# Performance work log

Measured on AMD Instinct MI355X. Metric: run time of the kernel, lower is better.

## Reference

```python
import jax, jax.numpy as jnp
import numpy as np

B, N, E, DJ, DE = 1024, 400, 128, 128, 128  # batch, nodes, edges, joint dim, edge dim (E must equal DJ and DE for BatchNorm1d on 3D input)
BN_EPS = 1e-5


def setup_inputs() -> dict:
    key = jax.random.key(0)
    ks = jax.random.split(key, 8)
    gout = jax.random.normal(ks[0], (B, N, DJ), dtype=jnp.float32)
    eout = jax.random.normal(ks[1], (B, E, DE), dtype=jnp.float32)
    start_shift = jax.random.uniform(ks[2], (B, E, N), dtype=jnp.float32)
    end_shift = jax.random.uniform(ks[3], (B, E, N), dtype=jnp.float32)
    # Linear params: nn.init.normal_(std=0.001), bias 0
    W1 = 0.001 * jax.random.normal(ks[4], (DJ, 2 * DJ), dtype=jnp.float32)
    b1 = jnp.zeros((DJ,), dtype=jnp.float32)
    W2 = 0.001 * jax.random.normal(ks[5], (DE, DJ), dtype=jnp.float32)
    b2 = jnp.zeros((DE,), dtype=jnp.float32)
    # BatchNorm affine params: weight=1, bias=0
    g1 = jnp.ones((DJ,), dtype=jnp.float32)
    beta1 = jnp.zeros((DJ,), dtype=jnp.float32)
    g2 = jnp.ones((DE,), dtype=jnp.float32)
    beta2 = jnp.zeros((DE,), dtype=jnp.float32)
    return {"gout": gout, "eout": eout, "start_shift": start_shift, "end_shift": end_shift,
            "W1": W1, "b1": b1, "W2": W2, "b2": b2,
            "g1": g1, "beta1": beta1, "g2": g2, "beta2": beta2}


def batchnorm1d(x, gamma, beta):
    # PyTorch BatchNorm1d on 3D input: channels at dim 1, biased variance over dims (0, 2)
    mean = jnp.mean(x, axis=(0, 2), keepdims=True)
    var = jnp.mean(jnp.square(x - mean), axis=(0, 2), keepdims=True)
    xhat = (x - mean) * jax.lax.rsqrt(var + BN_EPS)
    return xhat * gamma[None, :, None] + beta[None, :, None]


def reference(gout, eout, start_shift, end_shift, W1, b1, W2, b2, g1, beta1, g2, beta2):
    # node -> edge gather via dense shift matmuls: [B,E,N] @ [B,N,DJ] -> [B,E,DJ]
    start_nodes = jnp.matmul(start_shift, gout)
    end_nodes = jnp.matmul(end_shift, gout)
    x = jnp.concatenate([start_nodes, end_nodes], axis=2)  # [B, E, 2*DJ]
    h = jnp.einsum('bef,df->bed', x, W1) + b1  # Linear(2*DJ -> DJ)
    h = jax.nn.relu(batchnorm1d(h, g1, beta1))
    h = jnp.einsum('bed,od->beo', h, W2) + b2  # Linear(DJ -> DE)
    res = batchnorm1d(h, g2, beta2)
    return jax.nn.relu(eout + res)
```

## Files before the change

kernel.cpp:

```cpp
#include <hip/hip_runtime.h>
#include <stdint.h>

#define BB 1024
#define NN 400
#define EE 128
#define DD 128
#define NSLOT 64
#define GTS2 232
#define KH0 224
#define KH1 192

typedef float f32x4 __attribute__((ext_vector_type(4)));
typedef short bf16x8 __attribute__((ext_vector_type(8)));

__device__ __forceinline__ short f2bf(float f) {
    uint32_t u = __builtin_bit_cast(uint32_t, f);
    u += 0x7fffu + ((u >> 16) & 1u);
    return (short)(u >> 16);
}

__device__ __forceinline__ float bf2f(short s) {
    return __builtin_bit_cast(float, (uint32_t)((uint16_t)s) << 16);
}

__device__ __forceinline__ bf16x8 cvt8(const f32x4 a, const f32x4 b) {
    bf16x8 r;
    r[0] = f2bf(a[0]); r[1] = f2bf(a[1]); r[2] = f2bf(a[2]); r[3] = f2bf(a[3]);
    r[4] = f2bf(b[0]); r[5] = f2bf(b[1]); r[6] = f2bf(b[2]); r[7] = f2bf(b[3]);
    return r;
}

__global__ __launch_bounds__(256)
void k0_cvtw(const float* __restrict__ W1, const float* __restrict__ W2,
             unsigned short* __restrict__ W1b, unsigned short* __restrict__ W2b)
{
    int i = blockIdx.x * 256 + threadIdx.x;
    if (i < 32768) W1b[i] = (unsigned short)f2bf(W1[i]);
    if (i < 16384) W2b[i] = (unsigned short)f2bf(W2[i]);
}

__global__ __launch_bounds__(1024, 8)
void k1_gemm(const float* __restrict__ gout, const float* __restrict__ ss,
             const float* __restrict__ es, const unsigned short* __restrict__ W1b,
             const float* __restrict__ b1, unsigned short* __restrict__ h,
             float* __restrict__ stats1)
{
    __shared__ short lds[32768];
    short* GT = lds;
    short* Ps = lds;

    const int b   = blockIdx.x;
    const int t   = threadIdx.x;
    const int w   = t >> 6;
    const int l   = t & 63;
    const int l15 = l & 15;
    const int l4  = l >> 4;
    const int kkoff = l4 * 8;

    const int arow = (w & 7) * 16 + l15;
    const float* abase = ((w < 8) ? ss : es) + ((size_t)b * EE + arow) * NN;

    f32x4 pa0 = *(const f32x4*)(abase + kkoff);
    f32x4 pa1 = *(const f32x4*)(abase + kkoff + 4);
    f32x4 pb0 = *(const f32x4*)(abase + 32 + kkoff);
    f32x4 pb1 = *(const f32x4*)(abase + 32 + kkoff + 4);

    const float* gb = gout + (size_t)b * NN * DD + (t & 127);
    auto stage = [&](int koff, int nq) {
        const int qb = t >> 7;
        short* row = &GT[(t & 127) * GTS2];
        for (int q = qb; q < nq; q += 8) {
            int kg = koff + 4 * q;
            float v0 = (kg     < NN) ? gb[(size_t)(kg)     * DD] : 0.f;
            float v1 = (kg + 1 < NN) ? gb[(size_t)(kg + 1) * DD] : 0.f;
            float v2 = (kg + 2 < NN) ? gb[(size_t)(kg + 2) * DD] : 0.f;
            float v3 = (kg + 3 < NN) ? gb[(size_t)(kg + 3) * DD] : 0.f;
            uint32_t lo = (uint32_t)(uint16_t)f2bf(v0) | ((uint32_t)(uint16_t)f2bf(v1) << 16);
            uint32_t hi = (uint32_t)(uint16_t)f2bf(v2) | ((uint32_t)(uint16_t)f2bf(v3) << 16);
            *(uint64_t*)&row[4 * q] = ((uint64_t)hi << 32) | lo;
        }
    };

    stage(0, KH0 / 4);
    __syncthreads();

    f32x4 acc[8];
#pragma unroll
    for (int cf = 0; cf < 8; ++cf) acc[cf] = f32x4{0.f, 0.f, 0.f, 0.f};

#pragma unroll
    for (int s = 0; s < 13; ++s) {
        if (s == 7) {
            __syncthreads();
            stage(KH0, KH1 / 4);
            __syncthreads();
        }
        bf16x8 a = cvt8(pa0, pa1);
        pa0 = pb0; pa1 = pb1;
        const int sn = s + 2;
        if (sn < 12) {
            pb0 = *(const f32x4*)(abase + sn * 32 + kkoff);
            pb1 = *(const f32x4*)(abase + sn * 32 + kkoff + 4);
        } else if (sn == 12) {
            int kk = 384 + kkoff;
            pb0 = f32x4{0.f, 0.f, 0.f, 0.f};
            pb1 = f32x4{0.f, 0.f, 0.f, 0.f};
            if (kk < NN)     pb0 = *(const f32x4*)(abase + kk);
            if (kk + 4 < NN) pb1 = *(const f32x4*)(abase + kk + 4);
        }
        const int k0 = (s < 7 ? s * 32 : (s - 7) * 32) + kkoff;
#pragma unroll
        for (int cf = 0; cf < 8; ++cf) {
            bf16x8 gf = *(const bf16x8*)&GT[(cf * 16 + l15) * GTS2 + k0];
            acc[cf] = __builtin_amdgcn_mfma_f32_16x16x32_bf16(a, gf, acc[cf], 0, 0, 0);
        }
    }
    __syncthreads();

#pragma unroll
    for (int cf = 0; cf < 8; ++cf)
#pragma unroll
        for (int r = 0; r < 4; ++r) {
            int row = w * 16 + l4 * 4 + r;
            int col = cf * 16 + l15;
            Ps[row * 128 + (((col >> 3) ^ (row & 7)) << 3) + (col & 7)] = f2bf(acc[cf][r]);
        }
    __syncthreads();

    const int mt = w >> 1;
    const int jh = w & 1;
    f32x4 acc2[4];
#pragma unroll
    for (int cf = 0; cf < 4; ++cf) acc2[cf] = f32x4{0.f, 0.f, 0.f, 0.f};

#pragma unroll
    for (int kf = 0; kf < 8; ++kf) {
        int roff = (kf >= 4) ? 128 : 0;
        int kcol = (kf & 3) * 32 + l4 * 8;
        int row  = roff + mt * 16 + l15;
        int cb   = kcol >> 3;
        bf16x8 xf = *(const bf16x8*)&Ps[row * 128 + ((cb ^ (row & 7)) << 3)];
#pragma unroll
        for (int cf = 0; cf < 4; ++cf) {
            int j = jh * 64 + cf * 16 + l15;
            bf16x8 wf = *(const bf16x8*)&W1b[(size_t)j * 256 + kf * 32 + l4 * 8];
            acc2[cf] = __builtin_amdgcn_mfma_f32_16x16x32_bf16(xf, wf, acc2[cf], 0, 0, 0);
        }
    }
    __syncthreads();

    float* red = (float*)lds;
    float s_r[4] = {0.f, 0.f, 0.f, 0.f};
    float q_r[4] = {0.f, 0.f, 0.f, 0.f};
#pragma unroll
    for (int cf = 0; cf < 4; ++cf) {
        float bv = b1[jh * 64 + cf * 16 + l15];
        f32x4 v = acc2[cf] + bv;
#pragma unroll
        for (int r = 0; r < 4; ++r) {
            int e = mt * 16 + l4 * 4 + r;
            h[((size_t)b * EE + e) * DD + jh * 64 + cf * 16 + l15] = (unsigned short)f2bf(v[r]);
            s_r[r] += v[r];
            q_r[r] += v[r] * v[r];
        }
    }
#pragma unroll
    for (int r = 0; r < 4; ++r) {
        float s = s_r[r], q = q_r[r];
        s += __shfl_xor(s, 1); s += __shfl_xor(s, 2); s += __shfl_xor(s, 4); s += __shfl_xor(s, 8);
        q += __shfl_xor(q, 1); q += __shfl_xor(q, 2); q += __shfl_xor(q, 4); q += __shfl_xor(q, 8);
        if (l15 == 0) {
            int e = mt * 16 + l4 * 4 + r;
            red[(e << 1) | jh]         = s;
            red[256 + ((e << 1) | jh)] = q;
        }
    }
    __syncthreads();
    if (t < 128) {
        float s = red[2 * t] + red[2 * t + 1];
        float q = red[256 + 2 * t] + red[256 + 2 * t + 1];
        int slot = b & (NSLOT - 1);
        atomicAdd(&stats1[slot * 256 + t], s);
        atomicAdd(&stats1[slot * 256 + 128 + t], q);
    }
}

__global__ __launch_bounds__(256, 4)
void k3_gemm(unsigned short* h, const unsigned short* __restrict__ W2b,
             const float* __restrict__ b2, const float* __restrict__ g1,
             const float* __restrict__ bt1,
             const float* __restrict__ stats1, float* __restrict__ stats2)
{
    __shared__ short Xs[128 * 128];
    __shared__ float sc[128];
    __shared__ float sh[128];
    const int b   = blockIdx.x;
    const int t   = threadIdx.x;
    const int w   = t >> 6;
    const int l15 = t & 15;
    const int l4  = (t >> 4) & 3;

    if (t < 128) {
        float sm = 0.f, sq = 0.f;
#pragma unroll 8
        for (int sl = 0; sl < NSLOT; ++sl) {
            sm += stats1[sl * 256 + t];
            sq += stats1[sl * 256 + 128 + t];
        }
        const float inv_n = 1.0f / (1024.0f * 128.0f);
        float m    = sm * inv_n;
        float var  = sq * inv_n - m * m;
        float rstd = rsqrtf(var + 1e-5f);
        float s    = rstd * g1[t];
        sc[t] = s;
        sh[t] = bt1[t] - m * s;
    }
    __syncthreads();

    {
        const int c8 = t & 15;
        const int eb = t >> 4;
#pragma unroll
        for (int p = 0; p < 8; ++p) {
            int e = eb + 16 * p;
            bf16x8 v8 = *(const bf16x8*)&h[((size_t)b * EE + e) * DD + c8 * 8];
            float s = sc[e], s0 = sh[e];
            bf16x8 o;
#pragma unroll
            for (int i = 0; i < 8; ++i)
                o[i] = f2bf(fmaxf(fmaf(bf2f(v8[i]), s, s0), 0.0f));
            *(bf16x8*)&Xs[e * 128 + ((c8 ^ (e & 7)) << 3)] = o;
        }
    }
    __syncthreads();

    f32x4 acc[8][2];
#pragma unroll
    for (int i = 0; i < 8; ++i) {
        acc[i][0] = f32x4{0.f, 0.f, 0.f, 0.f};
        acc[i][1] = f32x4{0.f, 0.f, 0.f, 0.f};
    }
#pragma unroll
    for (int kf = 0; kf < 4; ++kf) {
        const int k0 = kf * 32;
        const int cb = (k0 >> 3) + l4;
        bf16x8 af[8];
#pragma unroll
        for (int rf = 0; rf < 8; ++rf) {
            int row = rf * 16 + l15;
            af[rf] = *(const bf16x8*)&Xs[row * 128 + ((cb ^ (row & 7)) * 8)];
        }
#pragma unroll
        for (int cf = 0; cf < 2; ++cf) {
            int j = w * 32 + cf * 16 + l15;
            bf16x8 bfr = *(const bf16x8*)&W2b[(size_t)j * 128 + k0 + l4 * 8];
#pragma unroll
            for (int rf = 0; rf < 8; ++rf)
                acc[rf][cf] = __builtin_amdgcn_mfma_f32_16x16x32_bf16(af[rf], bfr, acc[rf][cf], 0, 0, 0);
        }
    }

    __syncthreads();
    float* red = (float*)Xs;
    const float bj0 = b2[w * 32 + l15];
    const float bj1 = b2[w * 32 + 16 + l15];
    const int j0 = w * 32 + l15;
#pragma unroll
    for (int rf = 0; rf < 8; ++rf) {
        f32x4 v0 = acc[rf][0] + bj0;
        f32x4 v1 = acc[rf][1] + bj1;
        int elb = rf * 16 + l4 * 4;
#pragma unroll
        for (int r = 0; r < 4; ++r) {
            unsigned short* op = h + (size_t)(b * EE + elb + r) * DD;
            op[j0]      = (unsigned short)f2bf(v0[r]);
            op[j0 + 16] = (unsigned short)f2bf(v1[r]);
            float s = v0[r] + v1[r];
            float q = v0[r] * v0[r] + v1[r] * v1[r];
            s += __shfl_xor(s, 1); s += __shfl_xor(s, 2); s += __shfl_xor(s, 4); s += __shfl_xor(s, 8);
            q += __shfl_xor(q, 1); q += __shfl_xor(q, 2); q += __shfl_xor(q, 4); q += __shfl_xor(q, 8);
            if (l15 == 0) {
                red[(elb + r) * 4 + w]       = s;
                red[512 + (elb + r) * 4 + w] = q;
            }
        }
    }
    __syncthreads();
    if (t < 128) {
        float s = red[t * 4] + red[t * 4 + 1] + red[t * 4 + 2] + red[t * 4 + 3];
        float q = red[512 + t * 4] + red[512 + t * 4 + 1] + red[512 + t * 4 + 2] + red[512 + t * 4 + 3];
        int slot = b & (NSLOT - 1);
        atomicAdd(&stats2[slot * 256 + t], s);
        atomicAdd(&stats2[slot * 256 + 128 + t], q);
    }
}

__global__ __launch_bounds__(256)
void k5_final(const unsigned short* __restrict__ h2, const float* __restrict__ eout,
              const float* __restrict__ g2, const float* __restrict__ bt2,
              float* __restrict__ out, const float* __restrict__ stats2)
{
    __shared__ float sc[128];
    __shared__ float sh[128];
    const int t = threadIdx.x;
    if (t < 128) {
        float sm = 0.f, sq = 0.f;
#pragma unroll 8
        for (int sl = 0; sl < NSLOT; ++sl) {
            sm += stats2[sl * 256 + t];
            sq += stats2[sl * 256 + 128 + t];
        }
        const float inv_n = 1.0f / (1024.0f * 128.0f);
        float m    = sm * inv_n;
        float var  = sq * inv_n - m * m;
        float rstd = rsqrtf(var + 1e-5f);
        float s    = rstd * g2[t];
        sc[t] = s;
        sh[t] = bt2[t] - m * s;
    }
    __syncthreads();

    const int total8 = BB * EE * DD / 8;
    for (int i8 = blockIdx.x * blockDim.x + t; i8 < total8; i8 += gridDim.x * blockDim.x) {
        int e = (i8 >> 4) & 127;
        bf16x8 v8 = *(const bf16x8*)(h2 + (size_t)i8 * 8);
        f32x4 u0 = *(const f32x4*)(eout + (size_t)i8 * 8);
        f32x4 u1 = *(const f32x4*)(eout + (size_t)i8 * 8 + 4);
        float s = sc[e], s0 = sh[e];
        f32x4 o0, o1;
#pragma unroll
        for (int i = 0; i < 4; ++i) {
            o0[i] = fmaxf(u0[i] + fmaf(bf2f(v8[i]), s, s0), 0.0f);
            o1[i] = fmaxf(u1[i] + fmaf(bf2f(v8[i + 4]), s, s0), 0.0f);
        }
        *(f32x4*)(out + (size_t)i8 * 8)     = o0;
        *(f32x4*)(out + (size_t)i8 * 8 + 4) = o1;
    }
}

extern "C" void kernel_launch(void* const* d_in, const int* in_sizes, int n_in,
                              void* d_out, int out_size, void* d_ws, size_t ws_size,
                              hipStream_t stream)
{
    const float* gout  = (const float*)d_in[0];
    const float* eout  = (const float*)d_in[1];
    const float* ss    = (const float*)d_in[2];
    const float* es    = (const float*)d_in[3];
    const float* W1    = (const float*)d_in[4];
    const float* b1    = (const float*)d_in[5];
    const float* W2    = (const float*)d_in[6];
    const float* b2    = (const float*)d_in[7];
    const float* g1    = (const float*)d_in[8];
    const float* bt1   = (const float*)d_in[9];
    const float* g2    = (const float*)d_in[10];
    const float* bt2   = (const float*)d_in[11];

    float* stats1 = (float*)d_ws;
    float* stats2 = stats1 + NSLOT * 256;
    unsigned short* W1b = (unsigned short*)(stats2 + NSLOT * 256);
    unsigned short* W2b = W1b + 32768;
    unsigned short* h   = W2b + 16384;
    float* out    = (float*)d_out;

    hipMemsetAsync((void*)stats1, 0, 2 * NSLOT * 256 * sizeof(float), stream);
    k0_cvtw<<<dim3(128), dim3(256), 0, stream>>>(W1, W2, W1b, W2b);
    k1_gemm<<<dim3(BB), dim3(1024), 0, stream>>>(gout, ss, es, W1b, b1, h, stats1);
    k3_gemm<<<dim3(BB), dim3(256), 0, stream>>>(h, W2b, b2, g1, bt1, stats1, stats2);
    k5_final<<<dim3(2048), dim3(256), 0, stream>>>(h, eout, g2, bt2, out, stats2);
}
```

Before: 272.8 us.

## Split node-gather GEMM and W1 linear into two kernels via global scratch

The fused k1 kernel is split into two. k1a stages the whole transposed gout tile (all 400 nodes) into a larger LDS buffer in one pass, which removes the mid-loop restage and its barriers. It then writes the bf16 start/end products to global scratch, borrowing the output buffer. A new k1b kernel with 256 threads reloads those products and runs the W1 linear with a wider per-wave tile, then computes the BN1 statistics. This trades an extra 64KB-per-batch global round trip and one more launch for simpler staging and different occupancy. The larger LDS footprint of k1a (about 106KB) may limit how many blocks fit per CU.

```diff
diff --git a/kernel.cpp b/kernel.cpp
--- a/kernel.cpp
+++ b/kernel.cpp
@@ -6,9 +6,7 @@
 #define EE 128
 #define DD 128
 #define NSLOT 64
-#define GTS2 232
-#define KH0 224
-#define KH1 192
+#define GTS 424
 
 typedef float f32x4 __attribute__((ext_vector_type(4)));
 typedef short bf16x8 __attribute__((ext_vector_type(8)));
@@ -39,15 +37,13 @@
     if (i < 16384) W2b[i] = (unsigned short)f2bf(W2[i]);
 }
 
-__global__ __launch_bounds__(1024, 8)
-void k1_gemm(const float* __restrict__ gout, const float* __restrict__ ss,
-             const float* __restrict__ es, const unsigned short* __restrict__ W1b,
-             const float* __restrict__ b1, unsigned short* __restrict__ h,
-             float* __restrict__ stats1)
-{
-    __shared__ short lds[32768];
+__global__ __launch_bounds__(1024, 1)
+void k1a_gemm(const float* __restrict__ gout, const float* __restrict__ ss,
+              const float* __restrict__ es, unsigned short* __restrict__ Pg)
+{
+    __shared__ short lds[54272];
     short* GT = lds;
-    short* Ps = lds;
+    short* Pl = lds;
 
     const int b   = blockIdx.x;
     const int t   = threadIdx.x;
@@ -65,12 +61,12 @@
     f32x4 pb0 = *(const f32x4*)(abase + 32 + kkoff);
     f32x4 pb1 = *(const f32x4*)(abase + 32 + kkoff + 4);
 
-    const float* gb = gout + (size_t)b * NN * DD + (t & 127);
-    auto stage = [&](int koff, int nq) {
+    {
+        const float* gb = gout + (size_t)b * NN * DD + (t & 127);
         const int qb = t >> 7;
-        short* row = &GT[(t & 127) * GTS2];
-        for (int q = qb; q < nq; q += 8) {
-            int kg = koff + 4 * q;
+        short* row = &GT[(t & 127) * GTS];
+        for (int q = qb; q < 106; q += 8) {
+            int kg = 4 * q;
             float v0 = (kg     < NN) ? gb[(size_t)(kg)     * DD] : 0.f;
             float v1 = (kg + 1 < NN) ? gb[(size_t)(kg + 1) * DD] : 0.f;
             float v2 = (kg + 2 < NN) ? gb[(size_t)(kg + 2) * DD] : 0.f;
@@ -79,9 +75,7 @@
             uint32_t hi = (uint32_t)(uint16_t)f2bf(v2) | ((uint32_t)(uint16_t)f2bf(v3) << 16);
             *(uint64_t*)&row[4 * q] = ((uint64_t)hi << 32) | lo;
         }
-    };
-
-    stage(0, KH0 / 4);
+    }
     __syncthreads();
 
     f32x4 acc[8];
@@ -90,11 +84,6 @@
 
 #pragma unroll
     for (int s = 0; s < 13; ++s) {
-        if (s == 7) {
-            __syncthreads();
-            stage(KH0, KH1 / 4);
-            __syncthreads();
-        }
         bf16x8 a = cvt8(pa0, pa1);
         pa0 = pb0; pa1 = pb1;
         const int sn = s + 2;
@@ -108,10 +97,10 @@
             if (kk < NN)     pb0 = *(const f32x4*)(abase + kk);
             if (kk + 4 < NN) pb1 = *(const f32x4*)(abase + kk + 4);
         }
-        const int k0 = (s < 7 ? s * 32 : (s - 7) * 32) + kkoff;
+        const int k0 = s * 32 + kkoff;
 #pragma unroll
         for (int cf = 0; cf < 8; ++cf) {
-            bf16x8 gf = *(const bf16x8*)&GT[(cf * 16 + l15) * GTS2 + k0];
+            bf16x8 gf = *(const bf16x8*)&GT[(cf * 16 + l15) * GTS + k0];
             acc[cf] = __builtin_amdgcn_mfma_f32_16x16x32_bf16(a, gf, acc[cf], 0, 0, 0);
         }
     }
@@ -123,62 +112,96 @@
         for (int r = 0; r < 4; ++r) {
             int row = w * 16 + l4 * 4 + r;
             int col = cf * 16 + l15;
-            Ps[row * 128 + (((col >> 3) ^ (row & 7)) << 3) + (col & 7)] = f2bf(acc[cf][r]);
-        }
-    __syncthreads();
-
-    const int mt = w >> 1;
-    const int jh = w & 1;
-    f32x4 acc2[4];
-#pragma unroll
-    for (int cf = 0; cf < 4; ++cf) acc2[cf] = f32x4{0.f, 0.f, 0.f, 0.f};
-
+            Pl[row * 128 + (((col >> 3) ^ (row & 7)) << 3) + (col & 7)] = f2bf(acc[cf][r]);
+        }
+    __syncthreads();
+
+    unsigned short* pg = Pg + (size_t)b * 32768;
+#pragma unroll
+    for (int i = 0; i < 4; ++i) {
+        int idx = i * 1024 + t;
+        bf16x8 v = *(const bf16x8*)&lds[idx * 8];
+        *(bf16x8*)&pg[idx * 8] = v;
+    }
+}
+
+__global__ __launch_bounds__(256, 2)
+void k1b_stage2(const unsigned short* __restrict__ Pg,
+                const unsigned short* __restrict__ W1b,
+                const float* __restrict__ b1, unsigned short* __restrict__ h,
+                float* __restrict__ stats1)
+{
+    __shared__ short Ps[32768];
+    const int b   = blockIdx.x;
+    const int t   = threadIdx.x;
+    const int w   = t >> 6;
+    const int l15 = t & 15;
+    const int l4  = (t >> 4) & 3;
+
+    const unsigned short* pg = Pg + (size_t)b * 32768;
+#pragma unroll
+    for (int i = 0; i < 16; ++i) {
+        int idx = i * 256 + t;
+        bf16x8 v = *(const bf16x8*)&pg[idx * 8];
+        *(bf16x8*)&Ps[idx * 8] = v;
+    }
+    __syncthreads();
+
+    f32x4 acc[8][2];
+#pragma unroll
+    for (int i = 0; i < 8; ++i) {
+        acc[i][0] = f32x4{0.f, 0.f, 0.f, 0.f};
+        acc[i][1] = f32x4{0.f, 0.f, 0.f, 0.f};
+    }
 #pragma unroll
     for (int kf = 0; kf < 8; ++kf) {
-        int roff = (kf >= 4) ? 128 : 0;
-        int kcol = (kf & 3) * 32 + l4 * 8;
-        int row  = roff + mt * 16 + l15;
-        int cb   = kcol >> 3;
-        bf16x8 xf = *(const bf16x8*)&Ps[row * 128 + ((cb ^ (row & 7)) << 3)];
-#pragma unroll
-        for (int cf = 0; cf < 4; ++cf) {
-            int j = jh * 64 + cf * 16 + l15;
+        const int roff = (kf >= 4) ? 128 : 0;
+        const int cb   = (kf & 3) * 4 + l4;
+        bf16x8 af[8];
+#pragma unroll
+        for (int rf = 0; rf < 8; ++rf) {
+            int row = roff + rf * 16 + l15;
+            af[rf] = *(const bf16x8*)&Ps[row * 128 + ((cb ^ (row & 7)) << 3)];
+        }
+#pragma unroll
+        for (int cf = 0; cf < 2; ++cf) {
+            int j = w * 32 + cf * 16 + l15;
             bf16x8 wf = *(const bf16x8*)&W1b[(size_t)j * 256 + kf * 32 + l4 * 8];
-            acc2[cf] = __builtin_amdgcn_mfma_f32_16x16x32_bf16(xf, wf, acc2[cf], 0, 0, 0);
-        }
-    }
-    __syncthreads();
-
-    float* red = (float*)lds;
-    float s_r[4] = {0.f, 0.f, 0.f, 0.f};
-    float q_r[4] = {0.f, 0.f, 0.f, 0.f};
-#pragma unroll
-    for (int cf = 0; cf < 4; ++cf) {
-        float bv = b1[jh * 64 + cf * 16 + l15];
-        f32x4 v = acc2[cf] + bv;
+#pragma unroll
+            for (int rf = 0; rf < 8; ++rf)
+                acc[rf][cf] = __builtin_amdgcn_mfma_f32_16x16x32_bf16(af[rf], wf, acc[rf][cf], 0, 0, 0);
+        }
+    }
+
+    __syncthreads();
+    float* red = (float*)Ps;
+    const float bj0 = b1[w * 32 + l15];
+    const float bj1 = b1[w * 32 + 16 + l15];
+    const int j0 = w * 32 + l15;
+#pragma unroll
+    for (int rf = 0; rf < 8; ++rf) {
+        f32x4 v0 = acc[rf][0] + bj0;
+        f32x4 v1 = acc[rf][1] + bj1;
+        int elb = rf * 16 + l4 * 4;
 #pragma unroll
         for (int r = 0; r < 4; ++r) {
-            int e = mt * 16 + l4 * 4 + r;
-            h[((size_t)b * EE + e) * DD + jh * 64 + cf * 16 + l15] = (unsigned short)f2bf(v[r]);
-            s_r[r] += v[r];
-            q_r[r] += v[r] * v[r];
-        }
-    }
-#pragma unroll
-    for (int r = 0; r < 4; ++r) {
-        float s = s_r[r], q = q_r[r];
-        s += __shfl_xor(s, 1); s += __shfl_xor(s, 2); s += __shfl_xor(s, 4); s += __shfl_xor(s, 8);
-        q += __shfl_xor(q, 1); q += __shfl_xor(q, 2); q += __shfl_xor(q, 4); q += __shfl_xor(q, 8);
-        if (l15 == 0) {
-            int e = mt * 16 + l4 * 4 + r;
-            red[(e << 1) | jh]         = s;
-            red[256 + ((e << 1) | jh)] = q;
+            unsigned short* hp = h + (size_t)(b * EE + elb + r) * DD;
+            hp[j0]      = (unsigned short)f2bf(v0[r]);
+            hp[j0 + 16] = (unsigned short)f2bf(v1[r]);
+            float s = v0[r] + v1[r];
+            float q = v0[r] * v0[r] + v1[r] * v1[r];
+            s += __shfl_xor(s, 1); s += __shfl_xor(s, 2); s += __shfl_xor(s, 4); s += __shfl_xor(s, 8);
+            q += __shfl_xor(q, 1); q += __shfl_xor(q, 2); q += __shfl_xor(q, 4); q += __shfl_xor(q, 8);
+            if (l15 == 0) {
+                red[(elb + r) * 4 + w]       = s;
+                red[512 + (elb + r) * 4 + w] = q;
+            }
         }
     }
     __syncthreads();
     if (t < 128) {
-        float s = red[2 * t] + red[2 * t + 1];
-        float q = red[256 + 2 * t] + red[256 + 2 * t + 1];
+        float s = red[t * 4] + red[t * 4 + 1] + red[t * 4 + 2] + red[t * 4 + 3];
+        float q = red[512 + t * 4] + red[512 + t * 4 + 1] + red[512 + t * 4 + 2] + red[512 + t * 4 + 3];
         int slot = b & (NSLOT - 1);
         atomicAdd(&stats1[slot * 256 + t], s);
         atomicAdd(&stats1[slot * 256 + 128 + t], q);
@@ -360,11 +383,13 @@
     unsigned short* W1b = (unsigned short*)(stats2 + NSLOT * 256);
     unsigned short* W2b = W1b + 32768;
     unsigned short* h   = W2b + 16384;
+    unsigned short* Pg  = (unsigned short*)d_out;
     float* out    = (float*)d_out;
 
     hipMemsetAsync((void*)stats1, 0, 2 * NSLOT * 256 * sizeof(float), stream);
     k0_cvtw<<<dim3(128), dim3(256), 0, stream>>>(W1, W2, W1b, W2b);
-    k1_gemm<<<dim3(BB), dim3(1024), 0, stream>>>(gout, ss, es, W1b, b1, h, stats1);
+    k1a_gemm<<<dim3(BB), dim3(1024), 0, stream>>>(gout, ss, es, Pg);
+    k1b_stage2<<<dim3(BB), dim3(256), 0, stream>>>(Pg, W1b, b1, h, stats1);
     k3_gemm<<<dim3(BB), dim3(256), 0, stream>>>(h, W2b, b2, g1, bt1, stats1, stats2);
     k5_final<<<dim3(2048), dim3(256), 0, stream>>>(h, eout, g2, bt2, out, stats2);
 }
```

New measurement: 262.8 us. 1.04x faster.

## Stream shift-matrix tiles into LDS via async global_load_lds triple buffering

Applied to the files above, without the earlier changes.

Replaces the register-prefetched loads of the start/end shift matrices with direct global-to-LDS asynchronous loads into a three-stage ring buffer, using vmcnt waits to overlap loads with the MFMA loop. The A tiles are XOR-swizzled in LDS to avoid bank conflicts, and LDS usage grows to about 154KB per block. This frees registers and hides memory latency, but it also changes the launch bound occupancy hint and adds reliance on waitcnt-based synchronization without barriers between waves. That is safe only because each wave reads only the data it loaded itself.

```diff
diff --git a/kernel.cpp b/kernel.cpp
--- a/kernel.cpp
+++ b/kernel.cpp
@@ -7,8 +7,6 @@
 #define DD 128
 #define NSLOT 64
 #define GTS2 232
-#define KH0 224
-#define KH1 192
 
 typedef float f32x4 __attribute__((ext_vector_type(4)));
 typedef short bf16x8 __attribute__((ext_vector_type(8)));
@@ -30,6 +28,12 @@
     return r;
 }
 
+__device__ __forceinline__ void gload16(const void* g, void* l) {
+    __builtin_amdgcn_global_load_lds(
+        (const __attribute__((address_space(1))) void*)g,
+        (__attribute__((address_space(3))) void*)l, 16, 0, 0);
+}
+
 __global__ __launch_bounds__(256)
 void k0_cvtw(const float* __restrict__ W1, const float* __restrict__ W2,
              unsigned short* __restrict__ W1b, unsigned short* __restrict__ W2b)
@@ -39,15 +43,16 @@
     if (i < 16384) W2b[i] = (unsigned short)f2bf(W2[i]);
 }
 
-__global__ __launch_bounds__(1024, 8)
+__global__ __launch_bounds__(1024, 1)
 void k1_gemm(const float* __restrict__ gout, const float* __restrict__ ss,
              const float* __restrict__ es, const unsigned short* __restrict__ W1b,
              const float* __restrict__ b1, unsigned short* __restrict__ h,
              float* __restrict__ stats1)
 {
-    __shared__ short lds[32768];
+    __shared__ short lds[78848];
     short* GT = lds;
-    short* Ps = lds;
+    float* Ab = (float*)&lds[29696];
+    short* Ps = &lds[29696];
 
     const int b   = blockIdx.x;
     const int t   = threadIdx.x;
@@ -55,18 +60,24 @@
     const int l   = t & 63;
     const int l15 = l & 15;
     const int l4  = l >> 4;
-    const int kkoff = l4 * 8;
-
-    const int arow = (w & 7) * 16 + l15;
-    const float* abase = ((w < 8) ? ss : es) + ((size_t)b * EE + arow) * NN;
-
-    f32x4 pa0 = *(const f32x4*)(abase + kkoff);
-    f32x4 pa1 = *(const f32x4*)(abase + kkoff + 4);
-    f32x4 pb0 = *(const f32x4*)(abase + 32 + kkoff);
-    f32x4 pb1 = *(const f32x4*)(abase + 32 + kkoff + 4);
+    const int jrow = l >> 3;
+    const int xchk = l & 7;
+
+    auto issueA = [&](int tile) {
+        float* dst = Ab + (tile % 3) * 8192 + w * 512;
+        const int k0 = tile * 32;
+#pragma unroll
+        for (int j = 0; j < 2; ++j) {
+            int r = w * 16 + j * 8 + jrow;
+            const float* base = ((r < 128) ? ss : es) + ((size_t)b * EE + (r & 127)) * NN;
+            int kc = k0 + ((xchk ^ (r & 7)) << 2);
+            if (kc >= NN) kc = 0;
+            gload16(base + kc, dst + j * 256);
+        }
+    };
 
     const float* gb = gout + (size_t)b * NN * DD + (t & 127);
-    auto stage = [&](int koff, int nq) {
+    auto stageGT = [&](int koff, int nq) {
         const int qb = t >> 7;
         short* row = &GT[(t & 127) * GTS2];
         for (int q = qb; q < nq; q += 8) {
@@ -81,7 +92,9 @@
         }
     };
 
-    stage(0, KH0 / 4);
+    issueA(0);
+    issueA(1);
+    stageGT(0, 56);
     __syncthreads();
 
     f32x4 acc[8];
@@ -92,23 +105,19 @@
     for (int s = 0; s < 13; ++s) {
         if (s == 7) {
             __syncthreads();
-            stage(KH0, KH1 / 4);
+            stageGT(224, 48);
             __syncthreads();
         }
-        bf16x8 a = cvt8(pa0, pa1);
-        pa0 = pb0; pa1 = pb1;
-        const int sn = s + 2;
-        if (sn < 12) {
-            pb0 = *(const f32x4*)(abase + sn * 32 + kkoff);
-            pb1 = *(const f32x4*)(abase + sn * 32 + kkoff + 4);
-        } else if (sn == 12) {
-            int kk = 384 + kkoff;
-            pb0 = f32x4{0.f, 0.f, 0.f, 0.f};
-            pb1 = f32x4{0.f, 0.f, 0.f, 0.f};
-            if (kk < NN)     pb0 = *(const f32x4*)(abase + kk);
-            if (kk + 4 < NN) pb1 = *(const f32x4*)(abase + kk + 4);
-        }
-        const int k0 = (s < 7 ? s * 32 : (s - 7) * 32) + kkoff;
+        if (s == 12) { asm volatile("s_waitcnt vmcnt(0)" ::: "memory"); }
+        else         { asm volatile("s_waitcnt vmcnt(2)" ::: "memory"); }
+        if (s + 2 < 13) issueA(s + 2);
+
+        const float* ap = Ab + (s % 3) * 8192 + w * 512 + l15 * 32;
+        f32x4 alo = *(const f32x4*)(ap + ((((2 * l4)     ^ (l15 & 7))) << 2));
+        f32x4 ahi = *(const f32x4*)(ap + ((((2 * l4 + 1) ^ (l15 & 7))) << 2));
+        bf16x8 a = cvt8(alo, ahi);
+
+        const int k0 = (s < 7 ? s * 32 : (s - 7) * 32) + l4 * 8;
 #pragma unroll
         for (int cf = 0; cf < 8; ++cf) {
             bf16x8 gf = *(const bf16x8*)&GT[(cf * 16 + l15) * GTS2 + k0];
@@ -136,9 +145,8 @@
 #pragma unroll
     for (int kf = 0; kf < 8; ++kf) {
         int roff = (kf >= 4) ? 128 : 0;
-        int kcol = (kf & 3) * 32 + l4 * 8;
         int row  = roff + mt * 16 + l15;
-        int cb   = kcol >> 3;
+        int cb   = (kf & 3) * 4 + l4;
         bf16x8 xf = *(const bf16x8*)&Ps[row * 128 + ((cb ^ (row & 7)) << 3)];
 #pragma unroll
         for (int cf = 0; cf < 4; ++cf) {
```

New measurement: 281.6 us. +3.2%, slower.

## Split k1 per-batch GEMM into two half-edge blocks with XCD-aware mapping

Applied to the files above, without the earlier changes.

Runs k1 as 2048 blocks of 512 threads instead of 1024 blocks of 1024. Each block handles 64 of the 128 edges for one batch, and blocks are remapped so consecutive indices land on the same XCD, which should keep a batch's gout in a shared L2. Smaller blocks and less LDS are meant to improve occupancy and tail behaviour. In exchange, each batch's gout tile is staged and converted twice, and MFMA sections get s_setprio raised.

```diff
diff --git a/kernel.cpp b/kernel.cpp
--- a/kernel.cpp
+++ b/kernel.cpp
@@ -7,8 +7,6 @@
 #define DD 128
 #define NSLOT 64
 #define GTS2 232
-#define KH0 224
-#define KH1 192
 
 typedef float f32x4 __attribute__((ext_vector_type(4)));
 typedef short bf16x8 __attribute__((ext_vector_type(8)));
@@ -39,17 +37,20 @@
     if (i < 16384) W2b[i] = (unsigned short)f2bf(W2[i]);
 }
 
-__global__ __launch_bounds__(1024, 8)
+__global__ __launch_bounds__(512, 4)
 void k1_gemm(const float* __restrict__ gout, const float* __restrict__ ss,
              const float* __restrict__ es, const unsigned short* __restrict__ W1b,
              const float* __restrict__ b1, unsigned short* __restrict__ h,
              float* __restrict__ stats1)
 {
-    __shared__ short lds[32768];
+    __shared__ short lds[29696];
     short* GT = lds;
     short* Ps = lds;
 
-    const int b   = blockIdx.x;
+    const int s_  = blockIdx.x;
+    const int wk  = (s_ & 7) * 256 + (s_ >> 3);
+    const int b   = wk >> 1;
+    const int e0  = (wk & 1) * 64;
     const int t   = threadIdx.x;
     const int w   = t >> 6;
     const int l   = t & 63;
@@ -57,8 +58,7 @@
     const int l4  = l >> 4;
     const int kkoff = l4 * 8;
 
-    const int arow = (w & 7) * 16 + l15;
-    const float* abase = ((w < 8) ? ss : es) + ((size_t)b * EE + arow) * NN;
+    const float* abase = ((w < 4) ? ss : es) + ((size_t)b * EE + e0 + (w & 3) * 16 + l15) * NN;
 
     f32x4 pa0 = *(const f32x4*)(abase + kkoff);
     f32x4 pa1 = *(const f32x4*)(abase + kkoff + 4);
@@ -66,10 +66,10 @@
     f32x4 pb1 = *(const f32x4*)(abase + 32 + kkoff + 4);
 
     const float* gb = gout + (size_t)b * NN * DD + (t & 127);
-    auto stage = [&](int koff, int nq) {
+    auto stageGT = [&](int koff, int nq) {
         const int qb = t >> 7;
         short* row = &GT[(t & 127) * GTS2];
-        for (int q = qb; q < nq; q += 8) {
+        for (int q = qb; q < nq; q += 4) {
             int kg = koff + 4 * q;
             float v0 = (kg     < NN) ? gb[(size_t)(kg)     * DD] : 0.f;
             float v1 = (kg + 1 < NN) ? gb[(size_t)(kg + 1) * DD] : 0.f;
@@ -81,7 +81,7 @@
         }
     };
 
-    stage(0, KH0 / 4);
+    stageGT(0, 56);
     __syncthreads();
 
     f32x4 acc[8];
@@ -92,7 +92,7 @@
     for (int s = 0; s < 13; ++s) {
         if (s == 7) {
             __syncthreads();
-            stage(KH0, KH1 / 4);
+            stageGT(224, 48);
             __syncthreads();
         }
         bf16x8 a = cvt8(pa0, pa1);
@@ -109,11 +109,13 @@
             if (kk + 4 < NN) pb1 = *(const f32x4*)(abase + kk + 4);
         }
         const int k0 = (s < 7 ? s * 32 : (s - 7) * 32) + kkoff;
+        __builtin_amdgcn_s_setprio(1);
 #pragma unroll
         for (int cf = 0; cf < 8; ++cf) {
             bf16x8 gf = *(const bf16x8*)&GT[(cf * 16 + l15) * GTS2 + k0];
             acc[cf] = __builtin_amdgcn_mfma_f32_16x16x32_bf16(a, gf, acc[cf], 0, 0, 0);
         }
+        __builtin_amdgcn_s_setprio(0);
     }
     __syncthreads();
 
@@ -121,7 +123,7 @@
     for (int cf = 0; cf < 8; ++cf)
 #pragma unroll
         for (int r = 0; r < 4; ++r) {
-            int row = w * 16 + l4 * 4 + r;
+            int row = ((w < 4) ? 0 : 64) + (w & 3) * 16 + l4 * 4 + r;
             int col = cf * 16 + l15;
             Ps[row * 128 + (((col >> 3) ^ (row & 7)) << 3) + (col & 7)] = f2bf(acc[cf][r]);
         }
@@ -135,10 +137,9 @@
 
 #pragma unroll
     for (int kf = 0; kf < 8; ++kf) {
-        int roff = (kf >= 4) ? 128 : 0;
-        int kcol = (kf & 3) * 32 + l4 * 8;
+        int roff = (kf >= 4) ? 64 : 0;
         int row  = roff + mt * 16 + l15;
-        int cb   = kcol >> 3;
+        int cb   = (kf & 3) * 4 + l4;
         bf16x8 xf = *(const bf16x8*)&Ps[row * 128 + ((cb ^ (row & 7)) << 3)];
 #pragma unroll
         for (int cf = 0; cf < 4; ++cf) {
@@ -159,7 +160,7 @@
 #pragma unroll
         for (int r = 0; r < 4; ++r) {
             int e = mt * 16 + l4 * 4 + r;
-            h[((size_t)b * EE + e) * DD + jh * 64 + cf * 16 + l15] = (unsigned short)f2bf(v[r]);
+            h[((size_t)b * EE + e0 + e) * DD + jh * 64 + cf * 16 + l15] = (unsigned short)f2bf(v[r]);
             s_r[r] += v[r];
             q_r[r] += v[r] * v[r];
         }
@@ -172,16 +173,16 @@
         if (l15 == 0) {
             int e = mt * 16 + l4 * 4 + r;
             red[(e << 1) | jh]         = s;
-            red[256 + ((e << 1) | jh)] = q;
-        }
-    }
-    __syncthreads();
-    if (t < 128) {
+            red[128 + ((e << 1) | jh)] = q;
+        }
+    }
+    __syncthreads();
+    if (t < 64) {
         float s = red[2 * t] + red[2 * t + 1];
-        float q = red[256 + 2 * t] + red[256 + 2 * t + 1];
-        int slot = b & (NSLOT - 1);
-        atomicAdd(&stats1[slot * 256 + t], s);
-        atomicAdd(&stats1[slot * 256 + 128 + t], q);
+        float q = red[128 + 2 * t] + red[128 + 2 * t + 1];
+        int slot = wk & (NSLOT - 1);
+        atomicAdd(&stats1[slot * 256 + e0 + t], s);
+        atomicAdd(&stats1[slot * 256 + 128 + e0 + t], q);
     }
 }
 
@@ -364,7 +365,7 @@
 
     hipMemsetAsync((void*)stats1, 0, 2 * NSLOT * 256 * sizeof(float), stream);
     k0_cvtw<<<dim3(128), dim3(256), 0, stream>>>(W1, W2, W1b, W2b);
-    k1_gemm<<<dim3(BB), dim3(1024), 0, stream>>>(gout, ss, es, W1b, b1, h, stats1);
+    k1_gemm<<<dim3(2 * BB), dim3(512), 0, stream>>>(gout, ss, es, W1b, b1, h, stats1);
     k3_gemm<<<dim3(BB), dim3(256), 0, stream>>>(h, W2b, b2, g1, bt1, stats1, stats2);
     k5_final<<<dim3(2048), dim3(256), 0, stream>>>(h, eout, g2, bt2, out, stats2);
 }
```

Result: no change. 275.4 us (+0.9%).
